# Optimization experiments

Measured on AMD Instinct MI355X. Metric: run time of the kernel, lower is better.

Reference implementation:

```python
import math
import jax, jax.numpy as jnp
import numpy as np

L, B, T, C, H = 12, 4, 1024, 1024, 16
D = C // H
EPS = 1e-5  # torch LayerNorm default


def setup_inputs() -> dict:
    key = jax.random.key(0)
    ks = jax.random.split(key, 8)
    s = 0.02
    return {
        "x": jax.random.normal(ks[0], (B, T, C), jnp.float32),
        "ln1_g": jnp.ones((L, C), jnp.float32),
        "ln1_b": jnp.zeros((L, C), jnp.float32),
        "attn_w": jax.random.normal(ks[1], (L, C, 3 * C), jnp.float32) * s,
        "attn_b": jnp.zeros((L, 3 * C), jnp.float32),
        "proj_w": jax.random.normal(ks[2], (L, C, C), jnp.float32) * s,
        "proj_b": jnp.zeros((L, C), jnp.float32),
        "ln2_g": jnp.ones((L, C), jnp.float32),
        "ln2_b": jnp.zeros((L, C), jnp.float32),
        "fc_w": jax.random.normal(ks[3], (L, C, 4 * C), jnp.float32) * s,
        "fc_b": jnp.zeros((L, 4 * C), jnp.float32),
        "fc2_w": jax.random.normal(ks[4], (L, 4 * C, C), jnp.float32) * s,
        "fc2_b": jnp.zeros((L, C), jnp.float32),
        "lnf_g": jnp.ones((C,), jnp.float32),
        "lnf_b": jnp.zeros((C,), jnp.float32),
    }


def layer_norm(x, g, b):
    m = jnp.mean(x, axis=-1, keepdims=True)
    v = jnp.var(x, axis=-1, keepdims=True)
    return (x - m) * jax.lax.rsqrt(v + EPS) * g + b


def new_gelu(x):
    # 0.5*x*(1+tanh(sqrt(2/pi)*(x+0.044715*x^3)))  (tanh-approx GELU)
    c = math.sqrt(2.0 / math.pi)
    return 0.5 * x * (1.0 + jnp.tanh(c * (x + 0.044715 * x ** 3)))


def block(x, p):
    ln1g, ln1b, aw, ab, pw, pb, ln2g, ln2b, fw, fb, f2w, f2b = p
    # causal self attention
    h = layer_norm(x, ln1g, ln1b)
    qkv = h @ aw + ab                                   # [B,T,3C]
    q, k, v = jnp.split(qkv, 3, axis=-1)
    q = q.reshape(B, T, H, D).transpose(0, 2, 1, 3)      # [B,H,T,D]
    k = k.reshape(B, T, H, D).transpose(0, 2, 1, 3)
    v = v.reshape(B, T, H, D).transpose(0, 2, 1, 3)
    att = jnp.einsum("bhqd,bhkd->bhqk", q, k) * (1.0 / math.sqrt(D))
    mask = jnp.tril(jnp.ones((T, T), dtype=bool))
    att = jnp.where(mask, att, -jnp.inf)
    att = jax.nn.softmax(att, axis=-1)
    y = jnp.einsum("bhqk,bhkd->bhqd", att, v)            # [B,H,T,D]
    y = y.transpose(0, 2, 1, 3).reshape(B, T, C)
    x = x + (y @ pw + pb)
    # MLP
    h = layer_norm(x, ln2g, ln2b)
    x = x + (new_gelu(h @ fw + fb) @ f2w + f2b)
    return x


def reference(x, ln1_g, ln1_b, attn_w, attn_b, proj_w, proj_b,
              ln2_g, ln2_b, fc_w, fc_b, fc2_w, fc2_b, lnf_g, lnf_b):
    params = (ln1_g, ln1_b, attn_w, attn_b, proj_w, proj_b,
              ln2_g, ln2_b, fc_w, fc_b, fc2_w, fc2_b)
    x, _ = jax.lax.scan(lambda c, p: (block(c, p), None), x, params)
    return layer_norm(x, lnf_g, lnf_b)
```

## Files before the change

### kernel.cpp

```cpp
#include <hip/hip_runtime.h>


typedef __bf16 bf16x8 __attribute__((ext_vector_type(8)));
typedef float f32x4 __attribute__((ext_vector_type(4)));
typedef unsigned short u16x8 __attribute__((ext_vector_type(8)));

__device__ __forceinline__ unsigned short f2b(float f) {
    union { float f; unsigned u; } x{f};
    unsigned r = x.u + 0x7FFF + ((x.u >> 16) & 1);
    return (unsigned short)(r >> 16);
}

__device__ __forceinline__ float gelu_f(float x) {
    float u = 0.7978845608028654f * (x + 0.044715f * x * x * x);
    float t = __expf(2.f * u);
    float th = 1.f - 2.f / (t + 1.f);
    return 0.5f * x * (1.f + th);
}

__device__ __forceinline__ void g2l16(const unsigned short* g, unsigned short* l) {
    __builtin_amdgcn_global_load_lds(
        (const __attribute__((address_space(1))) void*)g,
        (__attribute__((address_space(3))) void*)l, 16, 0, 0);
}

template <int BF16OUT>
__global__ __launch_bounds__(256) void ln_kernel(
    const float* __restrict__ x, const float* __restrict__ g,
    const float* __restrict__ bt, void* __restrict__ out) {
    const int row = blockIdx.x, tid = threadIdx.x;
    const float4 v = *(const float4*)(x + (size_t)row * 1024 + tid * 4);
    float s = v.x + v.y + v.z + v.w;
    float q = v.x * v.x + v.y * v.y + v.z * v.z + v.w * v.w;
    #pragma unroll
    for (int d = 1; d < 64; d <<= 1) { s += __shfl_xor(s, d); q += __shfl_xor(q, d); }
    __shared__ float ss[4], sq[4];
    const int w = tid >> 6;
    if ((tid & 63) == 0) { ss[w] = s; sq[w] = q; }
    __syncthreads();
    s = ss[0] + ss[1] + ss[2] + ss[3];
    q = sq[0] + sq[1] + sq[2] + sq[3];
    const float mean = s * (1.f / 1024.f);
    const float var = q * (1.f / 1024.f) - mean * mean;
    const float inv = rsqrtf(var + 1e-5f);
    const float4 gg = *(const float4*)(g + tid * 4);
    const float4 bb = *(const float4*)(bt + tid * 4);
    const float y0 = (v.x - mean) * inv * gg.x + bb.x;
    const float y1 = (v.y - mean) * inv * gg.y + bb.y;
    const float y2 = (v.z - mean) * inv * gg.z + bb.z;
    const float y3 = (v.w - mean) * inv * gg.w + bb.w;
    if (BF16OUT) {
        uint2 p;
        p.x = (unsigned)f2b(y0) | ((unsigned)f2b(y1) << 16);
        p.y = (unsigned)f2b(y2) | ((unsigned)f2b(y3) << 16);
        ((uint2*)out)[(size_t)row * 256 + tid] = p;
    } else {
        ((float4*)out)[(size_t)row * 256 + tid] = make_float4(y0, y1, y2, y3);
    }
}

__global__ __launch_bounds__(256) void wtrans_kernel(
    const float* __restrict__ W, unsigned short* __restrict__ Wt, int K, int N) {
    __shared__ float T[64][68];
    const int tid = threadIdx.x;
    const int n0 = blockIdx.x * 64, k0 = blockIdx.y * 64;
    #pragma unroll
    for (int r = 0; r < 4; ++r) {
        int li = tid + r * 256;
        int kk = li >> 4, nn = (li & 15) * 4;
        float4 v = *(const float4*)(W + (size_t)(k0 + kk) * N + n0 + nn);
        *(float4*)(&T[kk][nn]) = v;
    }
    __syncthreads();
    #pragma unroll
    for (int r = 0; r < 2; ++r) {
        int li = tid + r * 256;
        int nn = li >> 3, kc = li & 7;
        u16x8 t;
        #pragma unroll
        for (int j = 0; j < 8; ++j) t[j] = f2b(T[kc * 8 + j][nn]);
        *(u16x8*)(Wt + (size_t)(n0 + nn) * K + k0 + kc * 8) = t;
    }
}

template <int MODE>
__global__ __launch_bounds__(256) void gemm_kernel(
    const unsigned short* __restrict__ A, const unsigned short* __restrict__ Bt,
    const float* __restrict__ bias, const float* __restrict__ resid,
    void* __restrict__ out, int M, int N, int K) {
    __shared__ unsigned short As[128 * 64];
    __shared__ unsigned short Bs[128 * 64];
    const int tid = threadIdx.x, lane = tid & 63, w = tid >> 6;
    const int wm = w >> 1, wn = w & 1, lr = lane & 15, quad = lane >> 4;
    const int m0 = blockIdx.y * 128, n0 = blockIdx.x * 128;

    const int ar = lane >> 3;
    const int ac = (lane & 7) ^ ar;
    const unsigned short* Ag = A  + (size_t)(m0 + w * 32 + ar) * K + ac * 8;
    const unsigned short* Bg = Bt + (size_t)(n0 + w * 32 + ar) * K + ac * 8;

    f32x4 acc[4][4] = {};
    const int nk = K >> 6;
    for (int kt = 0; kt < nk; ++kt) {
        #pragma unroll
        for (int r = 0; r < 4; ++r) {
            g2l16(Ag + (size_t)(r * 8) * K, &As[(w * 32 + r * 8) * 64]);
            g2l16(Bg + (size_t)(r * 8) * K, &Bs[(w * 32 + r * 8) * 64]);
        }
        Ag += 64; Bg += 64;
        __syncthreads();
        #pragma unroll
        for (int s = 0; s < 2; ++s) {
            bf16x8 af[4], bf[4];
            #pragma unroll
            for (int i = 0; i < 4; ++i) {
                const int row = wm * 64 + i * 16 + lr;
                af[i] = *(const bf16x8*)(&As[row * 64 + ((((s << 2) + quad) ^ (lr & 7)) << 3)]);
            }
            #pragma unroll
            for (int j = 0; j < 4; ++j) {
                const int row = wn * 64 + j * 16 + lr;
                bf[j] = *(const bf16x8*)(&Bs[row * 64 + ((((s << 2) + quad) ^ (lr & 7)) << 3)]);
            }
            #pragma unroll
            for (int i = 0; i < 4; ++i)
                #pragma unroll
                for (int j = 0; j < 4; ++j)
                    acc[i][j] = __builtin_amdgcn_mfma_f32_16x16x32_bf16(af[i], bf[j], acc[i][j], 0, 0, 0);
        }
        __syncthreads();
    }
    #pragma unroll
    for (int i = 0; i < 4; ++i) {
        #pragma unroll
        for (int j = 0; j < 4; ++j) {
            const int gm0 = m0 + wm * 64 + i * 16 + quad * 4;
            const int gn = n0 + wn * 64 + j * 16 + lr;
            const float bb = bias[gn];
            #pragma unroll
            for (int r = 0; r < 4; ++r) {
                float v = acc[i][j][r] + bb;
                const size_t idx = (size_t)(gm0 + r) * N + gn;
                if (MODE == 2) {
                    ((float*)out)[idx] = resid[idx] + v;
                } else {
                    if (MODE == 1) v = gelu_f(v);
                    ((unsigned short*)out)[idx] = f2b(v);
                }
            }
        }
    }
}

__global__ __launch_bounds__(256) void attn_kernel(
    const unsigned short* __restrict__ qkv, unsigned short* __restrict__ y) {
    __shared__ unsigned short Ks[64 * 64];
    __shared__ unsigned short Vt[64 * 64];
    __shared__ unsigned short Ps[4][16 * 64];
    const int tid = threadIdx.x, lane = tid & 63, w = tid >> 6;
    const int lr = lane & 15, quad = lane >> 4;
    const int bx = blockIdx.x, bh = blockIdx.y;
    const int b = bh >> 4, h = bh & 15;
    const int q0 = bx * 64;
    const unsigned short* base = qkv + (size_t)b * 1024 * 3072 + h * 64;

    bf16x8 qf[2];
    {
        const int qr = q0 + w * 16 + lr;
        qf[0] = *(const bf16x8*)(base + (size_t)qr * 3072 + quad * 8);
        qf[1] = *(const bf16x8*)(base + (size_t)qr * 3072 + 32 + quad * 8);
    }
    float m_r[4], l_r[4];
    f32x4 o[4] = {};
    #pragma unroll
    for (int r = 0; r < 4; ++r) { m_r[r] = -3e38f; l_r[r] = 0.f; }

    const int nkt = bx + 1;
    for (int kt = 0; kt < nkt; ++kt) {
        #pragma unroll
        for (int r2 = 0; r2 < 2; ++r2) {
            int ci = tid + r2 * 256;
            int kr = ci >> 3, c = ci & 7;
            uint4 v = *(const uint4*)(base + (size_t)(kt * 64 + kr) * 3072 + 1024 + c * 8);
            *(uint4*)(&Ks[kr * 64 + ((c ^ (kr & 7)) << 3)]) = v;
        }
        #pragma unroll
        for (int r2 = 0; r2 < 2; ++r2) {
            int vr = (tid >> 3) + r2 * 32;
            int c = (tid & 7) * 8;
            u16x8 v = *(const u16x8*)(base + (size_t)(kt * 64 + vr) * 3072 + 2048 + c);
            #pragma unroll
            for (int j = 0; j < 8; ++j) {
                int d = c + j;
                Vt[d * 64 + (((vr >> 3) ^ (d & 7)) << 3) + (vr & 7)] = v[j];
            }
        }
        __syncthreads();

        f32x4 sf[4];
        #pragma unroll
        for (int jk = 0; jk < 4; ++jk) {
            f32x4 cf = {};
            #pragma unroll
            for (int s = 0; s < 2; ++s) {
                int krow = jk * 16 + lr;
                bf16x8 kf = *(const bf16x8*)(&Ks[krow * 64 + ((((s << 2) + quad) ^ (krow & 7)) << 3)]);
                cf = __builtin_amdgcn_mfma_f32_16x16x32_bf16(qf[s], kf, cf, 0, 0, 0);
            }
            #pragma unroll
            for (int r = 0; r < 4; ++r) sf[jk][r] = cf[r] * 0.125f;
        }
        if (kt == bx) {
            #pragma unroll
            for (int jk = 0; jk < 4; ++jk)
                #pragma unroll
                for (int r = 0; r < 4; ++r) {
                    int kcol = q0 + jk * 16 + lr;
                    int qr = q0 + w * 16 + quad * 4 + r;
                    if (kcol > qr) sf[jk][r] = -3e38f;
                }
        }
        #pragma unroll
        for (int r = 0; r < 4; ++r) {
            float mx = fmaxf(fmaxf(sf[0][r], sf[1][r]), fmaxf(sf[2][r], sf[3][r]));
            #pragma unroll
            for (int d = 1; d < 16; d <<= 1) mx = fmaxf(mx, __shfl_xor(mx, d));
            const float mnew = fmaxf(m_r[r], mx);
            const float alpha = __expf(m_r[r] - mnew);
            float rs = 0.f;
            #pragma unroll
            for (int jk = 0; jk < 4; ++jk) {
                float p = __expf(sf[jk][r] - mnew);
                sf[jk][r] = p;
                rs += p;
            }
            #pragma unroll
            for (int d = 1; d < 16; d <<= 1) rs += __shfl_xor(rs, d);
            l_r[r] = l_r[r] * alpha + rs;
            m_r[r] = mnew;
            #pragma unroll
            for (int jd = 0; jd < 4; ++jd) o[jd][r] *= alpha;
        }
        #pragma unroll
        for (int jk = 0; jk < 4; ++jk)
            #pragma unroll
            for (int r = 0; r < 4; ++r) {
                int row = quad * 4 + r;
                int col = jk * 16 + lr;
                Ps[w][row * 64 + (((col >> 3) ^ (row & 7)) << 3) + (col & 7)] = f2b(sf[jk][r]);
            }
        __syncthreads();
        #pragma unroll
        for (int s2 = 0; s2 < 2; ++s2) {
            bf16x8 pf = *(const bf16x8*)(&Ps[w][lr * 64 + ((((s2 << 2) + quad) ^ (lr & 7)) << 3)]);
            #pragma unroll
            for (int jd = 0; jd < 4; ++jd) {
                int dr = jd * 16 + lr;
                bf16x8 vf = *(const bf16x8*)(&Vt[dr * 64 + ((((s2 << 2) + quad) ^ (dr & 7)) << 3)]);
                o[jd] = __builtin_amdgcn_mfma_f32_16x16x32_bf16(pf, vf, o[jd], 0, 0, 0);
            }
        }
        __syncthreads();
    }
    #pragma unroll
    for (int jd = 0; jd < 4; ++jd)
        #pragma unroll
        for (int r = 0; r < 4; ++r) {
            int qr = q0 + w * 16 + quad * 4 + r;
            int d = jd * 16 + lr;
            y[((size_t)b * 1024 + qr) * 1024 + h * 64 + d] = f2b(o[jd][r] / l_r[r]);
        }
}

extern "C" void kernel_launch(void* const* d_in, const int* in_sizes, int n_in,
                              void* d_out, int out_size, void* d_ws, size_t ws_size,
                              hipStream_t stream) {
    const float* x      = (const float*)d_in[0];
    const float* ln1_g  = (const float*)d_in[1];
    const float* ln1_b  = (const float*)d_in[2];
    const float* attn_w = (const float*)d_in[3];
    const float* attn_b = (const float*)d_in[4];
    const float* proj_w = (const float*)d_in[5];
    const float* proj_b = (const float*)d_in[6];
    const float* ln2_g  = (const float*)d_in[7];
    const float* ln2_b  = (const float*)d_in[8];
    const float* fc_w   = (const float*)d_in[9];
    const float* fc_b   = (const float*)d_in[10];
    const float* fc2_w  = (const float*)d_in[11];
    const float* fc2_b  = (const float*)d_in[12];
    const float* lnf_g  = (const float*)d_in[13];
    const float* lnf_b  = (const float*)d_in[14];

    char* ws = (char*)d_ws;
    float* xf            = (float*)ws;
    unsigned short* hbuf = (unsigned short*)(ws + (16u << 20));
    unsigned short* qkvb = (unsigned short*)(ws + (24u << 20));
    unsigned short* yb   = (unsigned short*)(ws + (48u << 20));
    unsigned short* h2   = (unsigned short*)(ws + (56u << 20));
    unsigned short* wq   = (unsigned short*)(ws + (88u << 20));
    unsigned short* wp   = (unsigned short*)(ws + (94u << 20));
    unsigned short* wf   = (unsigned short*)(ws + (96u << 20));
    unsigned short* wf2  = (unsigned short*)(ws + (104u << 20));

    hipMemcpyAsync(xf, x, (size_t)4096 * 1024 * 4, hipMemcpyDeviceToDevice, stream);

    for (int l = 0; l < 12; ++l) {
        wtrans_kernel<<<dim3(48, 16), 256, 0, stream>>>(attn_w + (size_t)l * 1024 * 3072, wq, 1024, 3072);
        wtrans_kernel<<<dim3(16, 16), 256, 0, stream>>>(proj_w + (size_t)l * 1024 * 1024, wp, 1024, 1024);
        wtrans_kernel<<<dim3(64, 16), 256, 0, stream>>>(fc_w + (size_t)l * 1024 * 4096, wf, 1024, 4096);
        wtrans_kernel<<<dim3(16, 64), 256, 0, stream>>>(fc2_w + (size_t)l * 4096 * 1024, wf2, 4096, 1024);

        ln_kernel<1><<<4096, 256, 0, stream>>>(xf, ln1_g + l * 1024, ln1_b + l * 1024, hbuf);
        gemm_kernel<0><<<dim3(24, 32), 256, 0, stream>>>(hbuf, wq, attn_b + l * 3072, nullptr,
                                                         qkvb, 4096, 3072, 1024);
        attn_kernel<<<dim3(16, 64), 256, 0, stream>>>(qkvb, yb);
        gemm_kernel<2><<<dim3(8, 32), 256, 0, stream>>>(yb, wp, proj_b + l * 1024, xf,
                                                        xf, 4096, 1024, 1024);
        ln_kernel<1><<<4096, 256, 0, stream>>>(xf, ln2_g + l * 1024, ln2_b + l * 1024, hbuf);
        gemm_kernel<1><<<dim3(32, 32), 256, 0, stream>>>(hbuf, wf, fc_b + l * 4096, nullptr,
                                                         h2, 4096, 4096, 1024);
        gemm_kernel<2><<<dim3(8, 32), 256, 0, stream>>>(h2, wf2, fc2_b + l * 1024, xf,
                                                        xf, 4096, 1024, 4096);
    }
    ln_kernel<0><<<4096, 256, 0, stream>>>(xf, lnf_g, lnf_b, d_out);
}
```

Baseline: 4.377 ms.

## Batch weight transposes, enlarge attention Q tile, add 128x64 residual GEMM

Merges the four per-layer weight-transpose launches into one kernel that dispatches on block index, cutting launch count. The attention kernel now gives each block 128 query rows (32 per wave), so every K/V tile loaded into LDS is reused by twice as many rows. Fully masked subtiles are skipped, and exp2f with a log2(e) scale replaces __expf. The N=1024 residual GEMMs switch to a new 128x64-tile kernel that launches twice as many blocks to fill more CUs, at the cost of lower per-block reuse.

```diff
diff --git a/kernel.cpp b/kernel.cpp
--- a/kernel.cpp
+++ b/kernel.cpp
@@ -4,6 +4,8 @@
 typedef __bf16 bf16x8 __attribute__((ext_vector_type(8)));
 typedef float f32x4 __attribute__((ext_vector_type(4)));
 typedef unsigned short u16x8 __attribute__((ext_vector_type(8)));
+
+#define L2E 1.4426950408889634f
 
 __device__ __forceinline__ unsigned short f2b(float f) {
     union { float f; unsigned u; } x{f};
@@ -59,11 +61,20 @@
     }
 }
 
-__global__ __launch_bounds__(256) void wtrans_kernel(
-    const float* __restrict__ W, unsigned short* __restrict__ Wt, int K, int N) {
+struct WT4 {
+    const float *s0, *s1, *s2, *s3;
+    unsigned short *d0, *d1, *d2, *d3;
+};
+__global__ __launch_bounds__(256) void wtrans4_kernel(WT4 p) {
+    const int bid = blockIdx.x;
+    const float* W; unsigned short* Wt; int K, N, lid, nx;
+    if (bid < 768)       { W = p.s0; Wt = p.d0; K = 1024; N = 3072; lid = bid;        nx = 48; }
+    else if (bid < 1024) { W = p.s1; Wt = p.d1; K = 1024; N = 1024; lid = bid - 768;  nx = 16; }
+    else if (bid < 2048) { W = p.s2; Wt = p.d2; K = 1024; N = 4096; lid = bid - 1024; nx = 64; }
+    else                 { W = p.s3; Wt = p.d3; K = 4096; N = 1024; lid = bid - 2048; nx = 16; }
+    const int n0 = (lid % nx) * 64, k0 = (lid / nx) * 64;
     __shared__ float T[64][68];
     const int tid = threadIdx.x;
-    const int n0 = blockIdx.x * 64, k0 = blockIdx.y * 64;
     #pragma unroll
     for (int r = 0; r < 4; ++r) {
         int li = tid + r * 256;
@@ -152,30 +163,96 @@
     }
 }
 
+__global__ __launch_bounds__(256) void gemm64_kernel(
+    const unsigned short* __restrict__ A, const unsigned short* __restrict__ Bt,
+    const float* __restrict__ bias, const float* __restrict__ resid,
+    float* __restrict__ out, int M, int N, int K) {
+    __shared__ unsigned short As[128 * 64];
+    __shared__ unsigned short Bs[64 * 64];
+    const int tid = threadIdx.x, lane = tid & 63, w = tid >> 6;
+    const int lr = lane & 15, quad = lane >> 4;
+    const int m0 = blockIdx.y * 128, n0 = blockIdx.x * 64;
+
+    const int ar = lane >> 3;
+    const int ac = (lane & 7) ^ ar;
+    const unsigned short* Ag = A  + (size_t)(m0 + w * 32 + ar) * K + ac * 8;
+    const unsigned short* Bg = Bt + (size_t)(n0 + w * 16 + ar) * K + ac * 8;
+
+    f32x4 acc[2][4] = {};
+    const int nk = K >> 6;
+    for (int kt = 0; kt < nk; ++kt) {
+        #pragma unroll
+        for (int r = 0; r < 4; ++r)
+            g2l16(Ag + (size_t)(r * 8) * K, &As[(w * 32 + r * 8) * 64]);
+        #pragma unroll
+        for (int r = 0; r < 2; ++r)
+            g2l16(Bg + (size_t)(r * 8) * K, &Bs[(w * 16 + r * 8) * 64]);
+        Ag += 64; Bg += 64;
+        __syncthreads();
+        #pragma unroll
+        for (int s = 0; s < 2; ++s) {
+            bf16x8 af[2], bf[4];
+            #pragma unroll
+            for (int i = 0; i < 2; ++i) {
+                const int row = w * 32 + i * 16 + lr;
+                af[i] = *(const bf16x8*)(&As[row * 64 + ((((s << 2) + quad) ^ (lr & 7)) << 3)]);
+            }
+            #pragma unroll
+            for (int j = 0; j < 4; ++j) {
+                const int row = j * 16 + lr;
+                bf[j] = *(const bf16x8*)(&Bs[row * 64 + ((((s << 2) + quad) ^ (lr & 7)) << 3)]);
+            }
+            #pragma unroll
+            for (int i = 0; i < 2; ++i)
+                #pragma unroll
+                for (int j = 0; j < 4; ++j)
+                    acc[i][j] = __builtin_amdgcn_mfma_f32_16x16x32_bf16(af[i], bf[j], acc[i][j], 0, 0, 0);
+        }
+        __syncthreads();
+    }
+    #pragma unroll
+    for (int i = 0; i < 2; ++i) {
+        #pragma unroll
+        for (int j = 0; j < 4; ++j) {
+            const int gm0 = m0 + w * 32 + i * 16 + quad * 4;
+            const int gn = n0 + j * 16 + lr;
+            const float bb = bias[gn];
+            #pragma unroll
+            for (int r = 0; r < 4; ++r) {
+                const size_t idx = (size_t)(gm0 + r) * N + gn;
+                out[idx] = resid[idx] + acc[i][j][r] + bb;
+            }
+        }
+    }
+}
+
 __global__ __launch_bounds__(256) void attn_kernel(
     const unsigned short* __restrict__ qkv, unsigned short* __restrict__ y) {
     __shared__ unsigned short Ks[64 * 64];
     __shared__ unsigned short Vt[64 * 64];
-    __shared__ unsigned short Ps[4][16 * 64];
+    __shared__ unsigned short Ps[4][2][16 * 64];
     const int tid = threadIdx.x, lane = tid & 63, w = tid >> 6;
     const int lr = lane & 15, quad = lane >> 4;
     const int bx = blockIdx.x, bh = blockIdx.y;
     const int b = bh >> 4, h = bh & 15;
-    const int q0 = bx * 64;
+    const int q0 = bx * 128;
     const unsigned short* base = qkv + (size_t)b * 1024 * 3072 + h * 64;
 
-    bf16x8 qf[2];
-    {
-        const int qr = q0 + w * 16 + lr;
-        qf[0] = *(const bf16x8*)(base + (size_t)qr * 3072 + quad * 8);
-        qf[1] = *(const bf16x8*)(base + (size_t)qr * 3072 + 32 + quad * 8);
-    }
-    float m_r[4], l_r[4];
-    f32x4 o[4] = {};
-    #pragma unroll
-    for (int r = 0; r < 4; ++r) { m_r[r] = -3e38f; l_r[r] = 0.f; }
-
-    const int nkt = bx + 1;
+    bf16x8 qf[2][2];
+    #pragma unroll
+    for (int i = 0; i < 2; ++i) {
+        const int qr = q0 + w * 32 + i * 16 + lr;
+        qf[i][0] = *(const bf16x8*)(base + (size_t)qr * 3072 + quad * 8);
+        qf[i][1] = *(const bf16x8*)(base + (size_t)qr * 3072 + 32 + quad * 8);
+    }
+    float m_r[2][4], l_r[2][4];
+    f32x4 o[2][4] = {};
+    #pragma unroll
+    for (int i = 0; i < 2; ++i)
+        #pragma unroll
+        for (int r = 0; r < 4; ++r) { m_r[i][r] = -3e38f; l_r[i][r] = 0.f; }
+
+    const int nkt = 2 * bx + 2;
     for (int kt = 0; kt < nkt; ++kt) {
         #pragma unroll
         for (int r2 = 0; r2 < 2; ++r2) {
@@ -197,79 +274,85 @@
         }
         __syncthreads();
 
-        f32x4 sf[4];
-        #pragma unroll
-        for (int jk = 0; jk < 4; ++jk) {
-            f32x4 cf = {};
-            #pragma unroll
-            for (int s = 0; s < 2; ++s) {
-                int krow = jk * 16 + lr;
-                bf16x8 kf = *(const bf16x8*)(&Ks[krow * 64 + ((((s << 2) + quad) ^ (krow & 7)) << 3)]);
-                cf = __builtin_amdgcn_mfma_f32_16x16x32_bf16(qf[s], kf, cf, 0, 0, 0);
-            }
-            #pragma unroll
-            for (int r = 0; r < 4; ++r) sf[jk][r] = cf[r] * 0.125f;
-        }
-        if (kt == bx) {
+        #pragma unroll
+        for (int i = 0; i < 2; ++i) {
+            const int rowmin = q0 + w * 32 + i * 16;
+            if (kt * 64 > rowmin + 15) continue;
+            f32x4 sf[4];
+            #pragma unroll
+            for (int jk = 0; jk < 4; ++jk) {
+                f32x4 cf = {};
+                #pragma unroll
+                for (int s = 0; s < 2; ++s) {
+                    int krow = jk * 16 + lr;
+                    bf16x8 kf = *(const bf16x8*)(&Ks[krow * 64 + ((((s << 2) + quad) ^ (krow & 7)) << 3)]);
+                    cf = __builtin_amdgcn_mfma_f32_16x16x32_bf16(qf[i][s], kf, cf, 0, 0, 0);
+                }
+                #pragma unroll
+                for (int r = 0; r < 4; ++r) sf[jk][r] = cf[r] * 0.125f;
+            }
+            if (kt * 64 + 63 > rowmin) {
+                #pragma unroll
+                for (int jk = 0; jk < 4; ++jk)
+                    #pragma unroll
+                    for (int r = 0; r < 4; ++r) {
+                        int kcol = kt * 64 + jk * 16 + lr;
+                        int qr = rowmin + quad * 4 + r;
+                        if (kcol > qr) sf[jk][r] = -3e38f;
+                    }
+            }
+            #pragma unroll
+            for (int r = 0; r < 4; ++r) {
+                float mx = fmaxf(fmaxf(sf[0][r], sf[1][r]), fmaxf(sf[2][r], sf[3][r]));
+                #pragma unroll
+                for (int d = 1; d < 16; d <<= 1) mx = fmaxf(mx, __shfl_xor(mx, d));
+                const float mnew = fmaxf(m_r[i][r], mx);
+                const float alpha = exp2f((m_r[i][r] - mnew) * L2E);
+                float rs = 0.f;
+                #pragma unroll
+                for (int jk = 0; jk < 4; ++jk) {
+                    float p = exp2f((sf[jk][r] - mnew) * L2E);
+                    sf[jk][r] = p;
+                    rs += p;
+                }
+                #pragma unroll
+                for (int d = 1; d < 16; d <<= 1) rs += __shfl_xor(rs, d);
+                l_r[i][r] = l_r[i][r] * alpha + rs;
+                m_r[i][r] = mnew;
+                #pragma unroll
+                for (int jd = 0; jd < 4; ++jd) o[i][jd][r] *= alpha;
+            }
             #pragma unroll
             for (int jk = 0; jk < 4; ++jk)
                 #pragma unroll
                 for (int r = 0; r < 4; ++r) {
-                    int kcol = q0 + jk * 16 + lr;
-                    int qr = q0 + w * 16 + quad * 4 + r;
-                    if (kcol > qr) sf[jk][r] = -3e38f;
+                    int row = quad * 4 + r;
+                    int col = jk * 16 + lr;
+                    Ps[w][i][row * 64 + (((col >> 3) ^ (row & 7)) << 3) + (col & 7)] = f2b(sf[jk][r]);
                 }
-        }
-        #pragma unroll
-        for (int r = 0; r < 4; ++r) {
-            float mx = fmaxf(fmaxf(sf[0][r], sf[1][r]), fmaxf(sf[2][r], sf[3][r]));
-            #pragma unroll
-            for (int d = 1; d < 16; d <<= 1) mx = fmaxf(mx, __shfl_xor(mx, d));
-            const float mnew = fmaxf(m_r[r], mx);
-            const float alpha = __expf(m_r[r] - mnew);
-            float rs = 0.f;
-            #pragma unroll
-            for (int jk = 0; jk < 4; ++jk) {
-                float p = __expf(sf[jk][r] - mnew);
-                sf[jk][r] = p;
-                rs += p;
-            }
-            #pragma unroll
-            for (int d = 1; d < 16; d <<= 1) rs += __shfl_xor(rs, d);
-            l_r[r] = l_r[r] * alpha + rs;
-            m_r[r] = mnew;
-            #pragma unroll
-            for (int jd = 0; jd < 4; ++jd) o[jd][r] *= alpha;
-        }
-        #pragma unroll
-        for (int jk = 0; jk < 4; ++jk)
+            #pragma unroll
+            for (int s2 = 0; s2 < 2; ++s2) {
+                bf16x8 pf = *(const bf16x8*)(&Ps[w][i][lr * 64 + ((((s2 << 2) + quad) ^ (lr & 7)) << 3)]);
+                #pragma unroll
+                for (int jd = 0; jd < 4; ++jd) {
+                    int dr = jd * 16 + lr;
+                    bf16x8 vf = *(const bf16x8*)(&Vt[dr * 64 + ((((s2 << 2) + quad) ^ (dr & 7)) << 3)]);
+                    o[i][jd] = __builtin_amdgcn_mfma_f32_16x16x32_bf16(pf, vf, o[i][jd], 0, 0, 0);
+                }
+            }
+        }
+        __syncthreads();
+    }
+    #pragma unroll
+    for (int i = 0; i < 2; ++i)
+        #pragma unroll
+        for (int jd = 0; jd < 4; ++jd)
             #pragma unroll
             for (int r = 0; r < 4; ++r) {
-                int row = quad * 4 + r;
-                int col = jk * 16 + lr;
-                Ps[w][row * 64 + (((col >> 3) ^ (row & 7)) << 3) + (col & 7)] = f2b(sf[jk][r]);
-            }
-        __syncthreads();
-        #pragma unroll
-        for (int s2 = 0; s2 < 2; ++s2) {
-            bf16x8 pf = *(const bf16x8*)(&Ps[w][lr * 64 + ((((s2 << 2) + quad) ^ (lr & 7)) << 3)]);
-            #pragma unroll
-            for (int jd = 0; jd < 4; ++jd) {
-                int dr = jd * 16 + lr;
-                bf16x8 vf = *(const bf16x8*)(&Vt[dr * 64 + ((((s2 << 2) + quad) ^ (dr & 7)) << 3)]);
-                o[jd] = __builtin_amdgcn_mfma_f32_16x16x32_bf16(pf, vf, o[jd], 0, 0, 0);
-            }
-        }
-        __syncthreads();
-    }
-    #pragma unroll
-    for (int jd = 0; jd < 4; ++jd)
-        #pragma unroll
-        for (int r = 0; r < 4; ++r) {
-            int qr = q0 + w * 16 + quad * 4 + r;
-            int d = jd * 16 + lr;
-            y[((size_t)b * 1024 + qr) * 1024 + h * 64 + d] = f2b(o[jd][r] / l_r[r]);
-        }
+                int qr = q0 + w * 32 + i * 16 + quad * 4 + r;
+                int d = jd * 16 + lr;
+                y[((size_t)b * 1024 + qr) * 1024 + h * 64 + d] = f2b(o[i][jd][r] / l_r[i][r]);
+            }
 }
 
 extern "C" void kernel_launch(void* const* d_in, const int* in_sizes, int n_in,
@@ -305,21 +388,24 @@
     hipMemcpyAsync(xf, x, (size_t)4096 * 1024 * 4, hipMemcpyDeviceToDevice, stream);
 
     for (int l = 0; l < 12; ++l) {
-        wtrans_kernel<<<dim3(48, 16), 256, 0, stream>>>(attn_w + (size_t)l * 1024 * 3072, wq, 1024, 3072);
-        wtrans_kernel<<<dim3(16, 16), 256, 0, stream>>>(proj_w + (size_t)l * 1024 * 1024, wp, 1024, 1024);
-        wtrans_kernel<<<dim3(64, 16), 256, 0, stream>>>(fc_w + (size_t)l * 1024 * 4096, wf, 1024, 4096);
-        wtrans_kernel<<<dim3(16, 64), 256, 0, stream>>>(fc2_w + (size_t)l * 4096 * 1024, wf2, 4096, 1024);
+        WT4 p;
+        p.s0 = attn_w + (size_t)l * 1024 * 3072;
+        p.s1 = proj_w + (size_t)l * 1024 * 1024;
+        p.s2 = fc_w   + (size_t)l * 1024 * 4096;
+        p.s3 = fc2_w  + (size_t)l * 4096 * 1024;
+        p.d0 = wq; p.d1 = wp; p.d2 = wf; p.d3 = wf2;
+        wtrans4_kernel<<<3072, 256, 0, stream>>>(p);
 
         ln_kernel<1><<<4096, 256, 0, stream>>>(xf, ln1_g + l * 1024, ln1_b + l * 1024, hbuf);
         gemm_kernel<0><<<dim3(24, 32), 256, 0, stream>>>(hbuf, wq, attn_b + l * 3072, nullptr,
                                                          qkvb, 4096, 3072, 1024);
-        attn_kernel<<<dim3(16, 64), 256, 0, stream>>>(qkvb, yb);
-        gemm_kernel<2><<<dim3(8, 32), 256, 0, stream>>>(yb, wp, proj_b + l * 1024, xf,
+        attn_kernel<<<dim3(8, 64), 256, 0, stream>>>(qkvb, yb);
+        gemm64_kernel<<<dim3(16, 32), 256, 0, stream>>>(yb, wp, proj_b + l * 1024, xf,
                                                         xf, 4096, 1024, 1024);
         ln_kernel<1><<<4096, 256, 0, stream>>>(xf, ln2_g + l * 1024, ln2_b + l * 1024, hbuf);
         gemm_kernel<1><<<dim3(32, 32), 256, 0, stream>>>(hbuf, wf, fc_b + l * 4096, nullptr,
                                                          h2, 4096, 4096, 1024);
-        gemm_kernel<2><<<dim3(8, 32), 256, 0, stream>>>(h2, wf2, fc2_b + l * 1024, xf,
+        gemm64_kernel<<<dim3(16, 32), 256, 0, stream>>>(h2, wf2, fc2_b + l * 1024, xf,
                                                         xf, 4096, 1024, 4096);
     }
     ln_kernel<0><<<4096, 256, 0, stream>>>(xf, lnf_g, lnf_b, d_out);
```

Result: faster. 3.834 ms (-12.4%).
